# Kernel optimization log

Measured on AMD Instinct MI355X. Metric: run time of the kernel, lower is better.

The kernel has to match this reference:

```python
import jax, jax.numpy as jnp
import numpy as np

EPS = 1e-5
NEG_SLOPE = 0.01  # F.leaky_relu default


def setup_inputs() -> dict:
    key = jax.random.key(0)
    k1, k2, k3, k4 = jax.random.split(key, 4)
    b, c, n, p = 4, 32, 2048, 12
    out_size = 32
    n_agg, n_scal = 7, 3
    X = jax.random.normal(k1, (b, c, n, p), dtype=jnp.float32)
    A = jax.random.uniform(k2, (n, n), dtype=jnp.float32)  # dense weighted adjacency
    fan = n_agg * n_scal * c
    Theta = jax.random.normal(k3, (fan, out_size), dtype=jnp.float32) * np.float32(np.sqrt(2.0 / (fan + out_size)))
    stdv = np.float32(1.0 / np.sqrt(out_size))
    Bias = jax.random.uniform(k4, (out_size,), dtype=jnp.float32, minval=-stdv, maxval=stdv)
    return {"X": X, "A": A, "Theta": Theta, "Bias": Bias}


def _aggregate(Xp, A):
    # Xp: [b, p, n, c], A: [n, n]. One fused pass: all aggregators share A@(.) reductions.
    deg = jnp.sum(A, axis=1)                   # [n]
    d = jnp.maximum(deg, EPS)[:, None]         # [n, 1]
    agg = lambda M: jnp.einsum('nm,bpmc->bpnc', A, M)
    m1 = agg(Xp) / d                           # E[x_j]
    m2 = agg(Xp * Xp) / d                      # E[x_j^2]
    m3 = agg(Xp ** 3) / d                      # E[x_j^3]
    m4 = agg(Xp ** 4) / d                      # E[x_j^4]
    e_pos = jnp.exp(Xp)
    e_neg = jnp.exp(-Xp)
    softmax = agg(Xp * e_pos) / (agg(e_pos) + EPS)
    softmin = agg(Xp * e_neg) / (agg(e_neg) + EPS)
    var = jax.nn.relu(m2 - m1 * m1)
    std = jnp.sqrt(var + EPS)
    # distance: E_j[(x_i - x_j)^2] expanded via moments (no [n,n,c] intermediate)
    dist = Xp * Xp - 2.0 * Xp * m1 + m2
    # second moment of squared distance: E_j[(x_i - x_j)^4]
    ed2 = Xp ** 4 - 4.0 * Xp ** 3 * m1 + 6.0 * Xp ** 2 * m2 - 4.0 * Xp * m3 + m4
    d_std = jnp.sqrt(jax.nn.relu(ed2 - dist * dist) + EPS)
    # order matches aggregators list: softmin, softmax, normalized_mean, std, var, distance, d_std
    return jnp.concatenate([softmin, softmax, m1, std, var, dist, d_std], axis=-1)


def reference(X, A, Theta, Bias):
    # X: [b, c, n, p] -> [b, p, n, c]
    Xp = jnp.transpose(X, (0, 3, 2, 1))
    out = _aggregate(Xp, A)                    # [b, p, n, 7c]
    deg = jnp.sum(A, axis=1)
    logd = jnp.log(deg + 1.0)
    delta = jnp.mean(logd)                     # avg log-degree (PNA scaler normalizer)
    s = (logd / delta)[None, None, :, None]
    # scalers: identity, amplification, attenuation
    out = jnp.concatenate([out, out * s, out / jnp.maximum(s, EPS)], axis=-1)  # [b, p, n, 21c]
    out = jnp.einsum('bpnc,co->bpno', out, Theta) + Bias
    out = jnp.transpose(out, (0, 3, 2, 1))     # [b, o, n, p]
    # dropout is identity at inference (training=False)
    return jax.nn.leaky_relu(out, NEG_SLOPE)
```

## Files before the change

### kernel.cpp

```cpp
#include <hip/hip_runtime.h>
#include <hip/hip_bf16.h>
#include <cstdint>
#include <cstddef>

typedef unsigned short u16;
typedef unsigned long long u64;
typedef __bf16 bf16x8 __attribute__((ext_vector_type(8)));
typedef float f32x4 __attribute__((ext_vector_type(4)));
typedef unsigned int u32x4 __attribute__((ext_vector_type(4)));

#define EPSF 1e-5f

__device__ __forceinline__ float b2f(u16 u) {
  unsigned int i = ((unsigned int)u) << 16;
  return __builtin_bit_cast(float, i);
}
__device__ __forceinline__ u16 f2b(float f) {
  unsigned int u = __builtin_bit_cast(unsigned int, f);
  u = u + 0x7fffu + ((u >> 16) & 1u);
  return (u16)(u >> 16);
}

__device__ __forceinline__ void async_load16(const u16* g, u16* l) {
  __builtin_amdgcn_global_load_lds(
      (__attribute__((address_space(1))) void*)(g),
      (__attribute__((address_space(3))) void*)(l), 16, 0, 0);
}

__global__ __launch_bounds__(256) void prep_kernel(
    const void* __restrict__ X, const void* __restrict__ A,
    const void* __restrict__ Th, u16* __restrict__ Abf, u16* __restrict__ Ft,
    float* __restrict__ deg, float* __restrict__ logd, u16* __restrict__ ThT) {
  __shared__ int sbad;
  __shared__ float Xl[256 * 13];
  __shared__ float red[4];
  const int tid = threadIdx.x;
  if (tid == 0) sbad = 0;
  __syncthreads();
  {
    const u16* Xu = (const u16*)X;
    int bad = 0;
#pragma unroll
    for (int q = 0; q < 8; ++q) {
      float a = fabsf(b2f(Xu[q * 256 + tid]));
      if (!(a <= 1e4f)) bad = 1;
    }
    if (bad) atomicOr(&sbad, 1);
  }
  __syncthreads();
  const int isf32 = sbad;
  const int bid = blockIdx.x;

  if (bid < 2048) {
    const int row = bid;
    float s = 0.f;
    uint4 st;
    if (isf32) {
      const float4* Af = (const float4*)A + (size_t)row * 512 + tid * 2;
      float4 a = Af[0], b = Af[1];
      s = a.x + a.y + a.z + a.w + b.x + b.y + b.z + b.w;
      u16 o[8] = {f2b(a.x), f2b(a.y), f2b(a.z), f2b(a.w),
                  f2b(b.x), f2b(b.y), f2b(b.z), f2b(b.w)};
      st = *(const uint4*)o;
    } else {
      st = ((const uint4*)A)[(size_t)row * 256 + tid];
      const u16* o = (const u16*)&st;
#pragma unroll
      for (int k = 0; k < 8; ++k) s += b2f(o[k]);
    }
    *(uint4*)(Abf + (size_t)row * 2048 + tid * 8) = st;
#pragma unroll
    for (int off = 32; off > 0; off >>= 1) s += __shfl_down(s, off, 64);
    const int lane = tid & 63, w = tid >> 6;
    if (lane == 0) red[w] = s;
    __syncthreads();
    if (tid == 0) {
      float t = red[0] + red[1] + red[2] + red[3];
      deg[row] = t;
      logd[row] = logf(t + 1.f);
    }
  } else if (bid < 3072) {
    const int blk = bid - 2048;
    const int mc = blk & 7;
    const int ch = (blk >> 3) & 31;
    const int b  = blk >> 8;
    const size_t g0 = ((size_t)(b * 32 + ch) * 2048 + (size_t)mc * 256) * 12;
    if (isf32) {
      const float4* Xg = (const float4*)((const float*)X + g0);
#pragma unroll
      for (int q = 0; q < 3; ++q) {
        const int id = q * 256 + tid;
        const float4 v = Xg[id];
        const int j = id * 4, row = j / 12, col = j % 12;
        Xl[row * 13 + col]     = v.x;
        Xl[row * 13 + col + 1] = v.y;
        Xl[row * 13 + col + 2] = v.z;
        Xl[row * 13 + col + 3] = v.w;
      }
    } else {
      const u16* Xg = (const u16*)X + g0;
#pragma unroll
      for (int q = 0; q < 12; ++q) {
        const int id = q * 256 + tid;
        Xl[(id / 12) * 13 + id % 12] = b2f(Xg[id]);
      }
    }
    __syncthreads();
    for (int u = tid; u < 384; u += 256) {
      const int p = u >> 5;
      const int mg = u & 31;
      float x[8], e[8], en[8];
#pragma unroll
      for (int j = 0; j < 8; ++j) {
        x[j] = Xl[(mg * 8 + j) * 13 + p];
        e[j] = __expf(x[j]);
        en[j] = __expf(-x[j]);
      }
      const size_t cb = (size_t)(b * 12 + p) * 256 + ch;
      const int gmb = mc * 256 + mg * 8;
#pragma unroll
      for (int f = 0; f < 8; ++f) {
        u16 o[8];
#pragma unroll
        for (int j = 0; j < 8; ++j) {
          const float xx = x[j];
          const float x2 = xx * xx;
          float v;
          if      (f == 0) v = xx;
          else if (f == 1) v = x2;
          else if (f == 2) v = x2 * xx;
          else if (f == 3) v = x2 * x2;
          else if (f == 4) v = xx * e[j];
          else if (f == 5) v = e[j];
          else if (f == 6) v = xx * en[j];
          else             v = en[j];
          o[j] = f2b(v);
        }
        *(uint4*)(Ft + (cb + (size_t)f * 32) * 2048 + gmb) = *(const uint4*)o;
      }
    }
  } else {
    const int e = (bid - 3072) * 256 + tid;
    if (e < 21504) {
      const int k = e >> 5, o = e & 31;
      ThT[o * 672 + k] = isf32 ? f2b(((const float*)Th)[e]) : ((const u16*)Th)[e];
    }
  }
}

__global__ __launch_bounds__(256) void gemm_kernel(const u16* __restrict__ A,
                                                   const u16* __restrict__ Ft,
                                                   u16* __restrict__ Y) {
  __shared__ __attribute__((aligned(16))) u16 smem[2 * 128 * 64];
  u16* As = smem;
  u16* Bs = smem + 128 * 64;
  const int tid = threadIdx.x;
  const int wave = tid >> 6;
  const int lane = tid & 63;
  const int l15 = lane & 15;
  const int quad = lane >> 4;
  const int wm = wave >> 1;
  const int wn = wave & 1;

  const int i4 = blockIdx.x;
  const int xcd = i4 & 7;
  const int s4 = i4 >> 3;
  const int bm = (xcd >> 1) * 4 + (s4 & 3);
  const int bn = (xcd & 1) * 48 + (s4 >> 2);

  const int lrow = lane >> 3;
  const int schunk = (lane & 7) ^ lrow;
  const u16* gA = A  + (size_t)(bm * 128 + wave * 32 + lrow) * 2048 + schunk * 8;
  const u16* gB = Ft + (size_t)(bn * 128 + wave * 32 + lrow) * 2048 + schunk * 8;
  u16* lA = As + wave * 32 * 64 + lane * 8;
  u16* lB = Bs + wave * 32 * 64 + lane * 8;

  f32x4 acc[4][4];
#pragma unroll
  for (int i = 0; i < 4; ++i)
#pragma unroll
    for (int j = 0; j < 4; ++j) acc[i][j] = (f32x4){0.f, 0.f, 0.f, 0.f};

  for (int kk = 0; kk < 2048; kk += 64) {
    __syncthreads();
#pragma unroll
    for (int i = 0; i < 4; ++i) {
      async_load16(gA + (size_t)i * (8 * 2048) + kk, lA + i * (8 * 64));
      async_load16(gB + (size_t)i * (8 * 2048) + kk, lB + i * (8 * 64));
    }
    __syncthreads();
#pragma unroll
    for (int ks = 0; ks < 2; ++ks) {
      const int ca = ((ks * 4 + quad) ^ (l15 & 7)) * 8;
      bf16x8 af[4], bfr[4];
#pragma unroll
      for (int t = 0; t < 4; ++t)
        af[t] = *(const bf16x8*)(As + (wm * 64 + t * 16 + l15) * 64 + ca);
#pragma unroll
      for (int t = 0; t < 4; ++t)
        bfr[t] = *(const bf16x8*)(Bs + (wn * 64 + t * 16 + l15) * 64 + ca);
#pragma unroll
      for (int mt = 0; mt < 4; ++mt)
#pragma unroll
        for (int nt = 0; nt < 4; ++nt)
          acc[mt][nt] = __builtin_amdgcn_mfma_f32_16x16x32_bf16(af[mt], bfr[nt],
                                                                acc[mt][nt], 0, 0, 0);
    }
  }

  __syncthreads();
  u16* Cs = smem;
#pragma unroll
  for (int mt = 0; mt < 4; ++mt)
#pragma unroll
    for (int nt = 0; nt < 4; ++nt) {
      const int row = wm * 64 + mt * 16 + quad * 4;
      const int col = wn * 64 + nt * 16 + l15;
#pragma unroll
      for (int j = 0; j < 4; ++j)
        Cs[(row + j) * 128 + col] = f2b(acc[mt][nt][j]);
    }
  __syncthreads();
  const size_t ybase = (size_t)(bm * 128) * 12288 + (size_t)bn * 128;
#pragma unroll
  for (int q = 0; q < 8; ++q) {
    const int id = q * 256 + tid;
    const int r = id >> 4, c = (id & 15) * 8;
    __builtin_nontemporal_store(*(const u32x4*)(Cs + r * 128 + c),
                                (u32x4*)(Y + ybase + (size_t)r * 12288 + c));
  }
}

__global__ __launch_bounds__(256) void epilogue_kernel(
    const u16* __restrict__ Y, const u16* __restrict__ Fx,
    const float* __restrict__ deg, const float* __restrict__ logd,
    const u16* __restrict__ ThT, const void* __restrict__ Bias,
    void* __restrict__ out, const u16* __restrict__ Xu) {
  __shared__ __attribute__((aligned(16))) u16 Ys[32 * 264];
  __shared__ u16 Xs[32 * 33];
  __shared__ __attribute__((aligned(16))) u16 feats[32 * 680];
  __shared__ int sbad;
  __shared__ float red[4];
  const int tid = threadIdx.x;
  if (tid == 0) sbad = 0;
  __syncthreads();
  float ls = 0.f;
  {
    int bad = 0;
#pragma unroll
    for (int q = 0; q < 8; ++q) {
      float a = fabsf(b2f(Xu[q * 256 + tid]));
      if (!(a <= 1e4f)) bad = 1;
      ls += logd[q * 256 + tid];
    }
    if (bad) atomicOr(&sbad, 1);
  }
#pragma unroll
  for (int off = 32; off > 0; off >>= 1) ls += __shfl_down(ls, off, 64);
  if ((tid & 63) == 0) red[tid >> 6] = ls;
  __syncthreads();
  const int isf32 = sbad;
  const float delta = (red[0] + red[1] + red[2] + red[3]) * (1.0f / 2048.0f);

  const int nc = blockIdx.x;
  const int b  = blockIdx.y;
  const int pz = blockIdx.z;

  const int nl = tid >> 3;
  const int chg = tid & 7;
  const int inode = nc * 32 + nl;
  const float d = fmaxf(deg[inode], EPSF);
  const float rd = 1.0f / d;
  const float s = logd[inode] / delta;
  const float is = 1.0f / fmaxf(s, EPSF);

  const int wave = tid >> 6, lane = tid & 63;
  const int l15 = lane & 15, quad = lane >> 4;
  const int mt = wave >> 1, nt = wave & 1;
  const int o = nt * 16 + l15;
  const float bias = isf32 ? ((const float*)Bias)[o] : b2f(((const u16*)Bias)[o]);

  const int srr = tid >> 5 ? 0 : 0;
  float r[4][6];
  u32x4 yreg[4];
  u16 xreg[4];
  {
    const int bp0 = b * 12 + pz * 6;
#pragma unroll
    for (int q = 0; q < 4; ++q) {
      const int id = q * 256 + tid;
      const int rr = id >> 5, ck = id & 31;
      yreg[q] = __builtin_nontemporal_load(
          (const u32x4*)(Y + (size_t)(nc * 32 + rr) * 12288 + (size_t)bp0 * 256 + ck * 8));
      xreg[q] = Fx[(size_t)(bp0 * 256 + rr) * 2048 + nc * 32 + ck];
    }
  }

#pragma unroll
  for (int pp = 0; pp < 6; ++pp) {
    __syncthreads();
#pragma unroll
    for (int q = 0; q < 4; ++q) {
      const int id = q * 256 + tid;
      const int rr = id >> 5, ck = id & 31;
      *(u32x4*)(Ys + rr * 264 + ck * 8) = yreg[q];
      Xs[rr * 33 + ck] = xreg[q];
    }
    __syncthreads();
    if (pp < 5) {
      const int bpn = b * 12 + pz * 6 + pp + 1;
#pragma unroll
      for (int q = 0; q < 4; ++q) {
        const int id = q * 256 + tid;
        const int rr = id >> 5, ck = id & 31;
        yreg[q] = __builtin_nontemporal_load(
            (const u32x4*)(Y + (size_t)(nc * 32 + rr) * 12288 + (size_t)bpn * 256 + ck * 8));
        xreg[q] = Fx[(size_t)(bpn * 256 + rr) * 2048 + nc * 32 + ck];
      }
    }

    const u16* yr = Ys + nl * 264;
    float fv[7][4];
#pragma unroll
    for (int cc = 0; cc < 4; ++cc) {
      const int ch = chg * 4 + cc;
      const float m1 = b2f(yr[ch]) * rd;
      const float m2 = b2f(yr[32 + ch]) * rd;
      const float m3 = b2f(yr[64 + ch]) * rd;
      const float m4 = b2f(yr[96 + ch]) * rd;
      const float smx = b2f(yr[128 + ch]) / (b2f(yr[160 + ch]) + EPSF);
      const float smn = b2f(yr[192 + ch]) / (b2f(yr[224 + ch]) + EPSF);
      const float x = b2f(Xs[ch * 33 + nl]);
      const float var = fmaxf(m2 - m1 * m1, 0.f);
      const float stdv = sqrtf(var + EPSF);
      const float x2 = x * x, x3 = x2 * x, x4 = x2 * x2;
      const float dist = x2 - 2.f * x * m1 + m2;
      const float ed2 = x4 - 4.f * x3 * m1 + 6.f * x2 * m2 - 4.f * x * m3 + m4;
      const float dstd = sqrtf(fmaxf(ed2 - dist * dist, 0.f) + EPSF);
      fv[0][cc] = smn; fv[1][cc] = smx; fv[2][cc] = m1; fv[3][cc] = stdv;
      fv[4][cc] = var; fv[5][cc] = dist; fv[6][cc] = dstd;
    }
#pragma unroll
    for (int a = 0; a < 7; ++a) {
      u16 o0[4], o1[4], o2[4];
#pragma unroll
      for (int cc = 0; cc < 4; ++cc) {
        const float t = fv[a][cc];
        o0[cc] = f2b(t);
        o1[cc] = f2b(t * s);
        o2[cc] = f2b(t * is);
      }
      const int base = nl * 680 + a * 32 + chg * 4;
      *(u64*)(feats + base)       = *(const u64*)o0;
      *(u64*)(feats + base + 224) = *(const u64*)o1;
      *(u64*)(feats + base + 448) = *(const u64*)o2;
    }
    __syncthreads();

    f32x4 acc = (f32x4){0.f, 0.f, 0.f, 0.f};
#pragma unroll
    for (int kt = 0; kt < 21; ++kt) {
      bf16x8 a  = *(const bf16x8*)(feats + (mt * 16 + l15) * 680 + kt * 32 + quad * 8);
      bf16x8 bb = *(const bf16x8*)(ThT + (size_t)o * 672 + kt * 32 + quad * 8);
      acc = __builtin_amdgcn_mfma_f32_16x16x32_bf16(a, bb, acc, 0, 0, 0);
    }
#pragma unroll
    for (int j = 0; j < 4; ++j) r[j][pp] = acc[j];
  }

#pragma unroll
  for (int j = 0; j < 4; ++j) {
    const int node = mt * 16 + quad * 4 + j;
    const int ig = nc * 32 + node;
    const size_t oi = ((size_t)(b * 32 + o) * 2048 + ig) * 12 + pz * 6;
    float v[6];
#pragma unroll
    for (int k = 0; k < 6; ++k) {
      float t = r[j][k] + bias;
      v[k] = t > 0.f ? t : 0.01f * t;
    }
    if (isf32) {
      float* dst = (float*)out + oi;
      *(float2*)(dst)     = (float2){v[0], v[1]};
      *(float2*)(dst + 2) = (float2){v[2], v[3]};
      *(float2*)(dst + 4) = (float2){v[4], v[5]};
    } else {
      u16* dst = (u16*)out + oi;
#pragma unroll
      for (int k = 0; k < 6; ++k) dst[k] = f2b(v[k]);
    }
  }
}

extern "C" void kernel_launch(void* const* d_in, const int* in_sizes, int n_in,
                              void* d_out, int out_size, void* d_ws, size_t ws_size,
                              hipStream_t stream) {
  const void* X    = d_in[0];
  const void* A    = d_in[1];
  const void* Th   = d_in[2];
  const void* Bias = d_in[3];
  char* ws = (char*)d_ws;

  u16*   Ft   = (u16*)(ws);
  u16*   Y    = (u16*)(ws + 50331648);
  u16*   Abf  = (u16*)(ws + 100663296);
  float* deg  = (float*)(ws + 109051904);
  float* logd = (float*)(ws + 109060096);
  u16*   ThT  = (u16*)(ws + 109068288);

  prep_kernel<<<3156, 256, 0, stream>>>(X, A, Th, Abf, Ft, deg, logd, ThT);
  gemm_kernel<<<1536, 256, 0, stream>>>(Abf, Ft, Y);
  epilogue_kernel<<<dim3(64, 4, 2), 256, 0, stream>>>(Y, Ft, deg, logd, ThT,
                                                      Bias, d_out, (const u16*)X);
}
```

Measured before the change: 219.0 us.

## Fuse aggregator epilogue and Theta projection into the aggregation GEMM

Feature rows become interleaved per channel (the eight moment and exp features sit adjacent), so each GEMM tile holds every aggregate for 16 channels of one (b,p). The GEMM epilogue then computes the PNA features and scalers and multiplies them by a reordered, split Theta, writing partial fp32 outputs. This removes the large bf16 Y intermediate and the separate epilogue pass. A small transpose kernel sums the two channel halves, adds bias and applies leaky ReLU. The cost is extra work and synchronisation per GEMM block, plus an fp32 partial buffer.

```diff
diff --git a/kernel.cpp b/kernel.cpp
--- a/kernel.cpp
+++ b/kernel.cpp
@@ -30,7 +30,7 @@
 __global__ __launch_bounds__(256) void prep_kernel(
     const void* __restrict__ X, const void* __restrict__ A,
     const void* __restrict__ Th, u16* __restrict__ Abf, u16* __restrict__ Ft,
-    float* __restrict__ deg, float* __restrict__ logd, u16* __restrict__ ThT) {
+    float* __restrict__ deg, float* __restrict__ logd, u16* __restrict__ ThT2) {
   __shared__ int sbad;
   __shared__ float Xl[256 * 13];
   __shared__ float red[4];
@@ -116,7 +116,7 @@
         e[j] = __expf(x[j]);
         en[j] = __expf(-x[j]);
       }
-      const size_t cb = (size_t)(b * 12 + p) * 256 + ch;
+      const size_t cbase = (size_t)(b * 12 + p) * 256 + ch * 8;
       const int gmb = mc * 256 + mg * 8;
 #pragma unroll
       for (int f = 0; f < 8; ++f) {
@@ -136,22 +136,36 @@
           else             v = en[j];
           o[j] = f2b(v);
         }
-        *(uint4*)(Ft + (cb + (size_t)f * 32) * 2048 + gmb) = *(const uint4*)o;
+        *(uint4*)(Ft + (cbase + f) * 2048 + gmb) = *(const uint4*)o;
       }
     }
   } else {
     const int e = (bid - 3072) * 256 + tid;
     if (e < 21504) {
       const int k = e >> 5, o = e & 31;
-      ThT[o * 672 + k] = isf32 ? f2b(((const float*)Th)[e]) : ((const u16*)Th)[e];
-    }
-  }
-}
-
-__global__ __launch_bounds__(256) void gemm_kernel(const u16* __restrict__ A,
-                                                   const u16* __restrict__ Ft,
-                                                   u16* __restrict__ Y) {
+      const int sc = k / 224;
+      const int r2 = k - sc * 224;
+      const int a = r2 >> 5, ch = r2 & 31;
+      const int h = ch >> 4, cl = ch & 15;
+      const int kk = (a * 16 + cl) * 3 + sc;
+      const float v = isf32 ? ((const float*)Th)[e] : b2f(((const u16*)Th)[e]);
+      ThT2[(size_t)(h * 32 + o) * 352 + kk] = f2b(v);
+    }
+    if (bid == 3072) {
+      for (int t = tid; t < 1024; t += 256) {
+        const int h = t >> 9, rest = t & 511, o = rest >> 4, kp = 336 + (rest & 15);
+        ThT2[(size_t)(h * 32 + o) * 352 + kp] = 0;
+      }
+    }
+  }
+}
+
+__global__ __launch_bounds__(256) void gemm_fused_kernel(
+    const u16* __restrict__ A, const u16* __restrict__ Ft,
+    const float* __restrict__ deg, const float* __restrict__ logd,
+    const u16* __restrict__ ThT2, float* __restrict__ Yp) {
   __shared__ __attribute__((aligned(16))) u16 smem[2 * 128 * 64];
+  __shared__ float red4[4];
   u16* As = smem;
   u16* Bs = smem + 128 * 64;
   const int tid = threadIdx.x;
@@ -162,11 +176,22 @@
   const int wm = wave >> 1;
   const int wn = wave & 1;
 
+  float ls = 0.f;
+#pragma unroll
+  for (int q = 0; q < 8; ++q) ls += logd[q * 256 + tid];
+#pragma unroll
+  for (int off = 32; off > 0; off >>= 1) ls += __shfl_down(ls, off, 64);
+  if ((tid & 63) == 0) red4[tid >> 6] = ls;
+  __syncthreads();
+  const float delta = (red4[0] + red4[1] + red4[2] + red4[3]) * (1.0f / 2048.0f);
+
   const int i4 = blockIdx.x;
   const int xcd = i4 & 7;
   const int s4 = i4 >> 3;
   const int bm = (xcd >> 1) * 4 + (s4 & 3);
   const int bn = (xcd & 1) * 48 + (s4 >> 2);
+  const int h  = bn & 1;
+  const int bp = bn >> 1;
 
   const int lrow = lane >> 3;
   const int schunk = (lane & 7) ^ lrow;
@@ -207,187 +232,147 @@
                                                                 acc[mt][nt], 0, 0, 0);
     }
   }
-
-  __syncthreads();
-  u16* Cs = smem;
-#pragma unroll
-  for (int mt = 0; mt < 4; ++mt)
-#pragma unroll
-    for (int nt = 0; nt < 4; ++nt) {
-      const int row = wm * 64 + mt * 16 + quad * 4;
-      const int col = wn * 64 + nt * 16 + l15;
-#pragma unroll
-      for (int j = 0; j < 4; ++j)
-        Cs[(row + j) * 128 + col] = f2b(acc[mt][nt][j]);
-    }
-  __syncthreads();
-  const size_t ybase = (size_t)(bm * 128) * 12288 + (size_t)bn * 128;
-#pragma unroll
-  for (int q = 0; q < 8; ++q) {
-    const int id = q * 256 + tid;
-    const int r = id >> 4, c = (id & 15) * 8;
-    __builtin_nontemporal_store(*(const u32x4*)(Cs + r * 128 + c),
-                                (u32x4*)(Y + ybase + (size_t)r * 12288 + c));
-  }
-}
-
-__global__ __launch_bounds__(256) void epilogue_kernel(
-    const u16* __restrict__ Y, const u16* __restrict__ Fx,
-    const float* __restrict__ deg, const float* __restrict__ logd,
-    const u16* __restrict__ ThT, const void* __restrict__ Bias,
-    void* __restrict__ out, const u16* __restrict__ Xu) {
-  __shared__ __attribute__((aligned(16))) u16 Ys[32 * 264];
-  __shared__ u16 Xs[32 * 33];
-  __shared__ __attribute__((aligned(16))) u16 feats[32 * 680];
-  __shared__ int sbad;
-  __shared__ float red[4];
-  const int tid = threadIdx.x;
-  if (tid == 0) sbad = 0;
-  __syncthreads();
-  float ls = 0.f;
-  {
-    int bad = 0;
-#pragma unroll
-    for (int q = 0; q < 8; ++q) {
-      float a = fabsf(b2f(Xu[q * 256 + tid]));
-      if (!(a <= 1e4f)) bad = 1;
-      ls += logd[q * 256 + tid];
-    }
-    if (bad) atomicOr(&sbad, 1);
-  }
-#pragma unroll
-  for (int off = 32; off > 0; off >>= 1) ls += __shfl_down(ls, off, 64);
-  if ((tid & 63) == 0) red[tid >> 6] = ls;
-  __syncthreads();
-  const int isf32 = sbad;
-  const float delta = (red[0] + red[1] + red[2] + red[3]) * (1.0f / 2048.0f);
-
-  const int nc = blockIdx.x;
-  const int b  = blockIdx.y;
-  const int pz = blockIdx.z;
-
-  const int nl = tid >> 3;
-  const int chg = tid & 7;
-  const int inode = nc * 32 + nl;
-  const float d = fmaxf(deg[inode], EPSF);
-  const float rd = 1.0f / d;
-  const float s = logd[inode] / delta;
-  const float is = 1.0f / fmaxf(s, EPSF);
-
-  const int wave = tid >> 6, lane = tid & 63;
-  const int l15 = lane & 15, quad = lane >> 4;
-  const int mt = wave >> 1, nt = wave & 1;
-  const int o = nt * 16 + l15;
-  const float bias = isf32 ? ((const float*)Bias)[o] : b2f(((const u16*)Bias)[o]);
-
-  const int srr = tid >> 5 ? 0 : 0;
-  float r[4][6];
-  u32x4 yreg[4];
-  u16 xreg[4];
-  {
-    const int bp0 = b * 12 + pz * 6;
-#pragma unroll
-    for (int q = 0; q < 4; ++q) {
-      const int id = q * 256 + tid;
-      const int rr = id >> 5, ck = id & 31;
-      yreg[q] = __builtin_nontemporal_load(
-          (const u32x4*)(Y + (size_t)(nc * 32 + rr) * 12288 + (size_t)bp0 * 256 + ck * 8));
-      xreg[q] = Fx[(size_t)(bp0 * 256 + rr) * 2048 + nc * 32 + ck];
-    }
-  }
-
-#pragma unroll
-  for (int pp = 0; pp < 6; ++pp) {
-    __syncthreads();
-#pragma unroll
-    for (int q = 0; q < 4; ++q) {
-      const int id = q * 256 + tid;
-      const int rr = id >> 5, ck = id & 31;
-      *(u32x4*)(Ys + rr * 264 + ck * 8) = yreg[q];
-      Xs[rr * 33 + ck] = xreg[q];
-    }
-    __syncthreads();
-    if (pp < 5) {
-      const int bpn = b * 12 + pz * 6 + pp + 1;
-#pragma unroll
-      for (int q = 0; q < 4; ++q) {
-        const int id = q * 256 + tid;
-        const int rr = id >> 5, ck = id & 31;
-        yreg[q] = __builtin_nontemporal_load(
-            (const u32x4*)(Y + (size_t)(nc * 32 + rr) * 12288 + (size_t)bpn * 256 + ck * 8));
-        xreg[q] = Fx[(size_t)(bpn * 256 + rr) * 2048 + nc * 32 + ck];
-      }
-    }
-
-    const u16* yr = Ys + nl * 264;
-    float fv[7][4];
-#pragma unroll
-    for (int cc = 0; cc < 4; ++cc) {
-      const int ch = chg * 4 + cc;
-      const float m1 = b2f(yr[ch]) * rd;
-      const float m2 = b2f(yr[32 + ch]) * rd;
-      const float m3 = b2f(yr[64 + ch]) * rd;
-      const float m4 = b2f(yr[96 + ch]) * rd;
-      const float smx = b2f(yr[128 + ch]) / (b2f(yr[160 + ch]) + EPSF);
-      const float smn = b2f(yr[192 + ch]) / (b2f(yr[224 + ch]) + EPSF);
-      const float x = b2f(Xs[ch * 33 + nl]);
+  __syncthreads();
+
+  u16* Cs32 = smem;
+  u16* feats = smem + 32 * 144;
+#pragma unroll
+  for (int t = 0; t < 2; ++t) {
+    const int id = t * 256 + tid;
+    feats[(id >> 4) * 352 + 336 + (id & 15)] = 0;
+  }
+
+  const int mt2 = wave >> 1, nt2 = wave & 1;
+  const int oo = nt2 * 16 + l15;
+
+#pragma unroll
+  for (int c = 0; c < 4; ++c) {
+    if (wm == (c >> 1)) {
+#pragma unroll
+      for (int mtl = 0; mtl < 2; ++mtl) {
+        const int mt = 2 * (c & 1) + mtl;
+#pragma unroll
+        for (int nt = 0; nt < 4; ++nt) {
+          const int col = wn * 64 + nt * 16 + l15;
+#pragma unroll
+          for (int j = 0; j < 4; ++j) {
+            const int lr = mtl * 16 + quad * 4 + j;
+            float v;
+            if (mt == 0) v = acc[0][nt][j];
+            else if (mt == 1) v = acc[1][nt][j];
+            else if (mt == 2) v = acc[2][nt][j];
+            else v = acc[3][nt][j];
+            Cs32[lr * 144 + col] = f2b(v);
+          }
+        }
+      }
+    }
+    __syncthreads();
+#pragma unroll
+    for (int t = 0; t < 2; ++t) {
+      const int pt = t * 256 + tid;
+      const int n32 = pt >> 4, cl = pt & 15;
+      const int gi = bm * 128 + c * 32 + n32;
+      const float rd = 1.0f / fmaxf(deg[gi], EPSF);
+      const float s = logd[gi] / delta;
+      const float is = 1.0f / fmaxf(s, EPSF);
+      const u16* cr = Cs32 + n32 * 144 + cl * 8;
+      uint4 cv = *(const uint4*)cr;
+      const u16* cu = (const u16*)&cv;
+      const float m1 = b2f(cu[0]) * rd;
+      const float m2 = b2f(cu[1]) * rd;
+      const float m3 = b2f(cu[2]) * rd;
+      const float m4 = b2f(cu[3]) * rd;
+      const float smx = b2f(cu[4]) / (b2f(cu[5]) + EPSF);
+      const float smn = b2f(cu[6]) / (b2f(cu[7]) + EPSF);
+      const float x = b2f(Ft[(size_t)(bn * 128 + cl * 8) * 2048 + gi]);
       const float var = fmaxf(m2 - m1 * m1, 0.f);
       const float stdv = sqrtf(var + EPSF);
       const float x2 = x * x, x3 = x2 * x, x4 = x2 * x2;
       const float dist = x2 - 2.f * x * m1 + m2;
       const float ed2 = x4 - 4.f * x3 * m1 + 6.f * x2 * m2 - 4.f * x * m3 + m4;
       const float dstd = sqrtf(fmaxf(ed2 - dist * dist, 0.f) + EPSF);
-      fv[0][cc] = smn; fv[1][cc] = smx; fv[2][cc] = m1; fv[3][cc] = stdv;
-      fv[4][cc] = var; fv[5][cc] = dist; fv[6][cc] = dstd;
-    }
-#pragma unroll
-    for (int a = 0; a < 7; ++a) {
-      u16 o0[4], o1[4], o2[4];
-#pragma unroll
-      for (int cc = 0; cc < 4; ++cc) {
-        const float t = fv[a][cc];
-        o0[cc] = f2b(t);
-        o1[cc] = f2b(t * s);
-        o2[cc] = f2b(t * is);
-      }
-      const int base = nl * 680 + a * 32 + chg * 4;
-      *(u64*)(feats + base)       = *(const u64*)o0;
-      *(u64*)(feats + base + 224) = *(const u64*)o1;
-      *(u64*)(feats + base + 448) = *(const u64*)o2;
-    }
-    __syncthreads();
-
-    f32x4 acc = (f32x4){0.f, 0.f, 0.f, 0.f};
-#pragma unroll
-    for (int kt = 0; kt < 21; ++kt) {
-      bf16x8 a  = *(const bf16x8*)(feats + (mt * 16 + l15) * 680 + kt * 32 + quad * 8);
-      bf16x8 bb = *(const bf16x8*)(ThT + (size_t)o * 672 + kt * 32 + quad * 8);
-      acc = __builtin_amdgcn_mfma_f32_16x16x32_bf16(a, bb, acc, 0, 0, 0);
-    }
-#pragma unroll
-    for (int j = 0; j < 4; ++j) r[j][pp] = acc[j];
-  }
-
-#pragma unroll
-  for (int j = 0; j < 4; ++j) {
-    const int node = mt * 16 + quad * 4 + j;
-    const int ig = nc * 32 + node;
-    const size_t oi = ((size_t)(b * 32 + o) * 2048 + ig) * 12 + pz * 6;
-    float v[6];
-#pragma unroll
-    for (int k = 0; k < 6; ++k) {
-      float t = r[j][k] + bias;
-      v[k] = t > 0.f ? t : 0.01f * t;
+      const float f7[7] = {smn, smx, m1, stdv, var, dist, dstd};
+#pragma unroll
+      for (int a = 0; a < 7; ++a) {
+        const int kk = (a * 16 + cl) * 3;
+        const float v = f7[a];
+        feats[n32 * 352 + kk]     = f2b(v);
+        feats[n32 * 352 + kk + 1] = f2b(v * s);
+        feats[n32 * 352 + kk + 2] = f2b(v * is);
+      }
+    }
+    __syncthreads();
+    f32x4 pacc = (f32x4){0.f, 0.f, 0.f, 0.f};
+#pragma unroll
+    for (int kt = 0; kt < 11; ++kt) {
+      bf16x8 a  = *(const bf16x8*)(feats + (mt2 * 16 + l15) * 352 + kt * 32 + quad * 8);
+      bf16x8 bb = *(const bf16x8*)(ThT2 + (size_t)(h * 32 + oo) * 352 + kt * 32 + quad * 8);
+      pacc = __builtin_amdgcn_mfma_f32_16x16x32_bf16(a, bb, pacc, 0, 0, 0);
+    }
+    const int ibase = bm * 128 + c * 32 + mt2 * 16 + quad * 4;
+    __builtin_nontemporal_store(pacc,
+        (f32x4*)(Yp + ((size_t)(h * 48 + bp) * 32 + oo) * 2048 + ibase));
+    __syncthreads();
+  }
+}
+
+__global__ __launch_bounds__(256) void transpose_kernel(
+    const float* __restrict__ Yp, const void* __restrict__ Bias,
+    void* __restrict__ out, const u16* __restrict__ Xu) {
+  __shared__ float T[512 * 13];
+  __shared__ int sbad;
+  const int tid = threadIdx.x;
+  if (tid == 0) sbad = 0;
+  __syncthreads();
+  {
+    int bad = 0;
+#pragma unroll
+    for (int q = 0; q < 8; ++q) {
+      float a = fabsf(b2f(Xu[q * 256 + tid]));
+      if (!(a <= 1e4f)) bad = 1;
+    }
+    if (bad) atomicOr(&sbad, 1);
+  }
+  __syncthreads();
+  const int isf32 = sbad;
+
+  const int bid = blockIdx.x;
+  const int iq = bid & 3;
+  const int o  = (bid >> 2) & 31;
+  const int b  = bid >> 7;
+  const float bias = isf32 ? ((const float*)Bias)[o] : b2f(((const u16*)Bias)[o]);
+
+#pragma unroll
+  for (int p = 0; p < 12; ++p) {
+    const size_t base0 = ((size_t)((b * 12 + p)) * 32 + o) * 2048 + iq * 512;
+    const size_t base1 = ((size_t)(48 + b * 12 + p) * 32 + o) * 2048 + iq * 512;
+#pragma unroll
+    for (int t = 0; t < 2; ++t) {
+      const int ii = t * 256 + tid;
+      T[ii * 13 + p] = Yp[base0 + ii] + Yp[base1 + ii];
+    }
+  }
+  __syncthreads();
+  const size_t ob = ((size_t)(b * 32 + o) * 2048 + iq * 512) * 12;
+#pragma unroll
+  for (int t = 0; t < 2; ++t) {
+    const int r2 = tid * 2 + t;
+    float v[12];
+#pragma unroll
+    for (int p = 0; p < 12; ++p) {
+      float x = T[r2 * 13 + p] + bias;
+      v[p] = x > 0.f ? x : 0.01f * x;
     }
     if (isf32) {
-      float* dst = (float*)out + oi;
-      *(float2*)(dst)     = (float2){v[0], v[1]};
-      *(float2*)(dst + 2) = (float2){v[2], v[3]};
-      *(float2*)(dst + 4) = (float2){v[4], v[5]};
+      float* dst = (float*)out + ob + (size_t)r2 * 12;
+      *(float4*)(dst)     = (float4){v[0], v[1], v[2], v[3]};
+      *(float4*)(dst + 4) = (float4){v[4], v[5], v[6], v[7]};
+      *(float4*)(dst + 8) = (float4){v[8], v[9], v[10], v[11]};
     } else {
-      u16* dst = (u16*)out + oi;
-#pragma unroll
-      for (int k = 0; k < 6; ++k) dst[k] = f2b(v[k]);
+      u16* dst = (u16*)out + ob + (size_t)r2 * 12;
+#pragma unroll
+      for (int p = 0; p < 12; ++p) dst[p] = f2b(v[p]);
     }
   }
 }
@@ -402,14 +387,13 @@
   char* ws = (char*)d_ws;
 
   u16*   Ft   = (u16*)(ws);
-  u16*   Y    = (u16*)(ws + 50331648);
-  u16*   Abf  = (u16*)(ws + 100663296);
-  float* deg  = (float*)(ws + 109051904);
-  float* logd = (float*)(ws + 109060096);
-  u16*   ThT  = (u16*)(ws + 109068288);
-
-  prep_kernel<<<3156, 256, 0, stream>>>(X, A, Th, Abf, Ft, deg, logd, ThT);
-  gemm_kernel<<<1536, 256, 0, stream>>>(Abf, Ft, Y);
-  epilogue_kernel<<<dim3(64, 4, 2), 256, 0, stream>>>(Y, Ft, deg, logd, ThT,
-                                                      Bias, d_out, (const u16*)X);
-}
+  float* Yp   = (float*)(ws + 50331648);
+  u16*   Abf  = (u16*)(ws + 75497472);
+  float* deg  = (float*)(ws + 83886080);
+  float* logd = (float*)(ws + 83894272);
+  u16*   ThT2 = (u16*)(ws + 83902464);
+
+  prep_kernel<<<3156, 256, 0, stream>>>(X, A, Th, Abf, Ft, deg, logd, ThT2);
+  gemm_fused_kernel<<<1536, 256, 0, stream>>>(Abf, Ft, deg, logd, ThT2, Yp);
+  transpose_kernel<<<512, 256, 0, stream>>>(Yp, Bias, d_out, (const u16*)X);
+}
```

After: 361.8 us. +65.2%, slower.
